# Kernel tuning notes

Hardware: AMD Instinct MI355X
Metric: run time of the kernel (lower is better)

The kernel has to match this reference:

```python
import jax, jax.numpy as jnp
import numpy as np

# dims: d_model D, d_inner DI=2*D, d_state S, dt_rank R, conv kernel K, layers NL
D, DI, S, R, K, NL = 512, 1024, 16, 32, 4, 6
B, L = 4, 1024
EPS = 1e-5


def _ln(x, w, b):
    m = x.mean(-1, keepdims=True)
    v = ((x - m) ** 2).mean(-1, keepdims=True)
    return (x - m) * jax.lax.rsqrt(v + EPS) * w + b


def _causal_conv(x, w, b):
    # depthwise causal conv1d: x [B,L,DI], w [DI,K], left-pad K-1 (matches Conv1d(padding=K-1) then crop)
    xp = jnp.pad(x, ((0, 0), (K - 1, 0), (0, 0)))
    y = sum(xp[:, k:k + x.shape[1], :] * w[:, k] for k in range(K))
    return y + b


def _mamba(h, in_w, cw, cb, xp_w, dt_w, dt_b, A_log, Dp, out_w):
    # h: [B,L,D]
    xz = jnp.einsum('bld,ed->ble', h, in_w)        # [B,L,2*DI]
    x, z = jnp.split(xz, 2, axis=-1)
    x = jax.nn.silu(_causal_conv(x, cw, cb))       # [B,L,DI]
    dbc = jnp.einsum('bld,ed->ble', x, xp_w)       # [B,L,R+2S]
    dt_r, Bm, Cm = dbc[..., :R], dbc[..., R:R + S], dbc[..., R + S:]
    dt = jax.nn.softplus(jnp.einsum('blr,dr->bld', dt_r, dt_w) + dt_b)  # [B,L,DI]
    A = -jnp.exp(A_log)                            # [DI,S]

    def step(hst, inp):
        dt_t, B_t, C_t, x_t = inp                  # [B,DI],[B,S],[B,S],[B,DI]
        dA = jnp.exp(dt_t[..., None] * A)          # [B,DI,S]
        hst = dA * hst + (dt_t * x_t)[..., None] * B_t[:, None, :]
        y = jnp.einsum('bds,bs->bd', hst, C_t)
        return hst, y

    h0 = jnp.zeros((x.shape[0], DI, S), x.dtype)
    xs = (dt.transpose(1, 0, 2), Bm.transpose(1, 0, 2), Cm.transpose(1, 0, 2), x.transpose(1, 0, 2))
    _, ys = jax.lax.scan(step, h0, xs)
    y = ys.transpose(1, 0, 2) + x * Dp
    y = y * jax.nn.silu(z)
    return jnp.einsum('bld,ed->ble', y, out_w)     # [B,L,D]


def setup_inputs() -> dict:
    key = jax.random.key(0)
    ks = jax.random.split(key, 10)
    n = lambda k, shp, s: s * jax.random.normal(k, shp, jnp.float32)
    inp = {}
    inp['xs_pad'] = jax.random.normal(ks[0], (B, L, D), jnp.float32)
    inp['ilens'] = jax.random.randint(ks[1], (B,), 1, L + 1)
    inp['norm_w'] = jnp.ones((NL, D), jnp.float32)
    inp['norm_b'] = jnp.zeros((NL, D), jnp.float32)
    inp['in_proj_w'] = n(ks[2], (NL, 2 * DI, D), 0.02)
    inp['conv_w'] = n(ks[3], (NL, DI, K), 0.1)
    inp['conv_b'] = jnp.zeros((NL, DI), jnp.float32)
    inp['x_proj_w'] = n(ks[4], (NL, R + 2 * S, DI), 0.02)
    inp['dt_proj_w'] = n(ks[5], (NL, DI, R), 0.1)
    inp['dt_proj_b'] = n(ks[6], (NL, DI), 0.01)
    inp['A_log'] = jnp.log(jnp.broadcast_to(jnp.arange(1, S + 1, dtype=jnp.float32), (NL, DI, S)))
    inp['D_param'] = jnp.ones((NL, DI), jnp.float32)
    inp['out_proj_w'] = n(ks[7], (NL, D, DI), 0.02)
    inp['normf_w'] = jnp.ones((D,), jnp.float32)
    inp['normf_b'] = jnp.zeros((D,), jnp.float32)
    inp['after_w'] = jnp.ones((D,), jnp.float32)
    inp['after_b'] = jnp.zeros((D,), jnp.float32)
    return inp


def reference(xs_pad, ilens, norm_w, norm_b, in_proj_w, conv_w, conv_b, x_proj_w,
              dt_proj_w, dt_proj_b, A_log, D_param, out_proj_w,
              normf_w, normf_b, after_w, after_b):
    hidden = xs_pad
    residual = None
    for i in range(NL):
        residual = hidden + residual if residual is not None else hidden
        hn = _ln(residual, norm_w[i], norm_b[i])
        hidden = _mamba(hn, in_proj_w[i], conv_w[i], conv_b[i], x_proj_w[i],
                        dt_proj_w[i], dt_proj_b[i], A_log[i], D_param[i], out_proj_w[i])
    residual = hidden + residual
    out = _ln(residual, normf_w, normf_b)   # norm_f
    out = _ln(out, after_w, after_b)        # after_norm (normalize_before=True)
    olens = jnp.minimum(ilens, L)
    return out, olens
```

## Files before the change

kernel.cpp:

```cpp
#include <hip/hip_runtime.h>
#include <hip/hip_bf16.h>
#include <math.h>

#define D_   512
#define DI_  1024
#define S_   16
#define R_   32
#define KC_  4
#define NL_  6
#define B_   4
#define L_   1024
#define BL_  (B_*L_)
#define NC_  64
#define CL_  (L_/NC_)
#define BDI_ (B_*DI_)
#define LOG2E 1.44269504f
#define SKX  8
#define SKO  4

typedef __hip_bfloat16 bf16;
typedef __attribute__((ext_vector_type(8))) short bf16x8;
typedef __attribute__((ext_vector_type(4))) float f32x4;
typedef unsigned short u16;

#define QIDX(s, c, bd) (((size_t)(s) * NC_ + (c)) * BDI_ + (bd))

__device__ __forceinline__ float b2f(u16 u) {
  union { unsigned int i; float f; } x; x.i = ((unsigned int)u) << 16; return x.f;
}

__device__ __forceinline__ u16 f2bu(float f) {
  bf16 h = __float2bfloat16(f);
  return *(u16*)&h;
}

__device__ __forceinline__ float softplus_f(float v) {
  float e = __expf(-fabsf(v));
  return fmaxf(v, 0.f) + __logf(1.f + e);
}

__device__ __forceinline__ void gload16(const void* g, void* l) {
  __builtin_amdgcn_global_load_lds((const __attribute__((address_space(1))) void*)g,
                                   (__attribute__((address_space(3))) void*)l, 16, 0, 0);
}

#define N1_ (NL_*2*DI_*D_)
#define N2_ (N1_ + NL_*D_*DI_)
#define N3_ (N2_ + NL_*128*DI_)
#define N4_ (N3_ + NL_*DI_)
__global__ void setup_k(const float* __restrict__ in_w, const float* __restrict__ out_w,
                        const float* __restrict__ xp_w, const float* __restrict__ A_log,
                        bf16* __restrict__ inw_b, bf16* __restrict__ outw_b,
                        bf16* __restrict__ xpw_b,
                        float* __restrict__ an2b, float* __restrict__ ff,
                        float* __restrict__ an2f) {
  for (int i = blockIdx.x * blockDim.x + threadIdx.x; i < N4_; i += gridDim.x * blockDim.x) {
    if (i < N1_) {
      inw_b[i] = __float2bfloat16(in_w[i]);
    } else if (i < N2_) {
      int j = i - N1_;
      outw_b[j] = __float2bfloat16(out_w[j]);
    } else if (i < N3_) {
      int j = i - N2_;
      int c = j & (DI_ - 1);
      int r = (j >> 10) & 127;
      int l = j >> 17;
      float v = (r < 64) ? xp_w[((size_t)l * 64 + r) * DI_ + c] : 0.f;
      xpw_b[j] = __float2bfloat16(v);
    } else {
      int j = i - N3_;
      int d = j & (DI_ - 1);
      int l = j >> 10;
      float base = -expf(A_log[(size_t)j * S_]) * LOG2E;
      bool fast = true;
      #pragma unroll
      for (int s = 0; s < S_; ++s) {
        float a = -expf(A_log[(size_t)j * S_ + s]) * LOG2E;
        an2f[((size_t)l * S_ + s) * DI_ + d] = a;
        fast = fast && (fabsf(a - (float)(s + 1) * base) <= 1e-5f * fabsf(a));
      }
      an2b[j] = base;
      ff[j] = fast ? 1.f : 0.f;
    }
  }
}

__global__ __launch_bounds__(128) void addln_k(
    const float* __restrict__ x0, const u16* __restrict__ parts,
    u16* __restrict__ resid, const float* __restrict__ w, const float* __restrict__ b,
    bf16* __restrict__ hn, int first)
{
  __shared__ float red[4];
  const int row = blockIdx.x, t = threadIdx.x;
  const int lane = t & 63, wv = t >> 6;
  const size_t o = (size_t)row * D_ + t * 4;
  float4 v;
  if (first) {
    v = *(const float4*)(x0 + o);
  } else {
    const size_t ps = (size_t)BL_ * D_;
    v.x = 0.f; v.y = 0.f; v.z = 0.f; v.w = 0.f;
    #pragma unroll
    for (int p = 0; p < SKO; ++p) {
      ushort4 q = *(const ushort4*)(parts + p * ps + o);
      v.x += b2f(q.x); v.y += b2f(q.y); v.z += b2f(q.z); v.w += b2f(q.w);
    }
    ushort4 r = *(const ushort4*)(resid + o);
    v.x += b2f(r.x); v.y += b2f(r.y); v.z += b2f(r.z); v.w += b2f(r.w);
  }
  {
    ushort4 rw;
    rw.x = f2bu(v.x); rw.y = f2bu(v.y); rw.z = f2bu(v.z); rw.w = f2bu(v.w);
    *(ushort4*)(resid + o) = rw;
  }
  float s = v.x + v.y + v.z + v.w;
  float ss = v.x*v.x + v.y*v.y + v.z*v.z + v.w*v.w;
  #pragma unroll
  for (int o2 = 32; o2 > 0; o2 >>= 1) { s += __shfl_xor(s, o2); ss += __shfl_xor(ss, o2); }
  if (lane == 0) { red[wv * 2] = s; red[wv * 2 + 1] = ss; }
  __syncthreads();
  float S = red[0] + red[2], SS = red[1] + red[3];
  float m = S * (1.f / D_), var = SS * (1.f / D_) - m * m;
  float rs = rsqrtf(var + 1e-5f);
  float4 w4 = *(const float4*)(w + t * 4);
  float4 b4 = *(const float4*)(b + t * 4);
  bf16* o8 = hn + o;
  o8[0] = __float2bfloat16((v.x - m) * rs * w4.x + b4.x);
  o8[1] = __float2bfloat16((v.y - m) * rs * w4.y + b4.y);
  o8[2] = __float2bfloat16((v.z - m) * rs * w4.z + b4.z);
  o8[3] = __float2bfloat16((v.w - m) * rs * w4.w + b4.w);
}

__global__ __launch_bounds__(256) void gemm_bt(
    const bf16* __restrict__ A, int lda,
    const bf16* __restrict__ B, int ldb,
    bf16* __restrict__ Cb,
    int K, int Nact, int M, int epi)
{
  __shared__ __align__(16) bf16 As[128 * 32];
  __shared__ __align__(16) bf16 Bs[128 * 32];
  const int tid = threadIdx.x;
  const int wave = tid >> 6, lane = tid & 63;
  const int bm = blockIdx.x * 128, bn = blockIdx.y * 128;
  const int kz = blockIdx.z;
  const int Kc = K / gridDim.z;
  const int k0 = kz * Kc, k1 = k0 + Kc;
  const int wr = (wave >> 1) << 6, wc = (wave & 1) << 6;
  const int srow = lane >> 2, scg = lane & 3;
  const int rA = lane & 15, kq = (lane >> 4) << 3;
  f32x4 acc[4][4] = {};
  for (int kt = k0; kt < k1; kt += 32) {
    __syncthreads();
    #pragma unroll
    for (int p = 0; p < 2; ++p) {
      int chunk = wave * 2 + p;
      int row = (chunk << 4) + srow;
      gload16(A + (size_t)(bm + row) * lda + kt + scg * 8, &As[chunk * 512]);
      gload16(B + (size_t)(bn + row) * ldb + kt + scg * 8, &Bs[chunk * 512]);
    }
    __syncthreads();
    bf16x8 af[4], bq[4];
    #pragma unroll
    for (int m = 0; m < 4; ++m) af[m] = *(const bf16x8*)&As[(wr + m * 16 + rA) * 32 + kq];
    #pragma unroll
    for (int n = 0; n < 4; ++n) bq[n] = *(const bf16x8*)&Bs[(wc + n * 16 + rA) * 32 + kq];
    #pragma unroll
    for (int m = 0; m < 4; ++m)
      #pragma unroll
      for (int n = 0; n < 4; ++n)
        acc[m][n] = __builtin_amdgcn_mfma_f32_16x16x32_bf16(af[m], bq[n], acc[m][n], 0, 0, 0);
  }
  const int cr = (lane >> 4) << 2, cc = lane & 15;
  const size_t pbase = (epi == 1) ? (size_t)kz * M * Nact : 0;
  #pragma unroll
  for (int m = 0; m < 4; ++m)
    #pragma unroll
    for (int n = 0; n < 4; ++n) {
      int col = bn + wc + n * 16 + cc;
      if (col >= Nact) continue;
      #pragma unroll
      for (int j = 0; j < 4; ++j) {
        size_t row = (size_t)(bm + wr + m * 16 + cr + j);
        Cb[pbase + row * Nact + col] = __float2bfloat16(acc[m][n][j]);
      }
    }
}

__global__ __launch_bounds__(256) void conv_silu_k(
    const u16* __restrict__ xz, const float* __restrict__ cw, const float* __restrict__ cb,
    bf16* __restrict__ xcb)
{
  int g = blockIdx.x * 256 + threadIdx.x;
  int dq = g & (DI_ / 8 - 1);
  int bl = g >> 7;
  int l = bl & (L_ - 1), b = bl >> 10;
  int d = dq * 8;
  float a[8], wv[8][KC_];
  #pragma unroll
  for (int e = 0; e < 8; ++e) {
    float4 w4 = *(const float4*)(cw + (d + e) * KC_);
    wv[e][0] = w4.x; wv[e][1] = w4.y; wv[e][2] = w4.z; wv[e][3] = w4.w;
    a[e] = cb[d + e];
  }
  #pragma unroll
  for (int k = 0; k < KC_; ++k) {
    int lt = l + k - 3;
    if (lt < 0) continue;
    bf16x8 xv = *(const bf16x8*)(xz + (size_t)(b * L_ + lt) * (2 * DI_) + d);
    #pragma unroll
    for (int e = 0; e < 8; ++e) a[e] += b2f((u16)xv[e]) * wv[e][k];
  }
  bf16 o8[8];
  #pragma unroll
  for (int e = 0; e < 8; ++e) {
    float v = a[e] / (1.f + __expf(-a[e]));
    o8[e] = __float2bfloat16(v);
  }
  *(bf16x8*)(xcb + (size_t)bl * DI_ + d) = *(const bf16x8*)o8;
}


__global__ __launch_bounds__(256) void scanA_k(
    const u16* __restrict__ x, const u16* __restrict__ xpart,
    const float* __restrict__ dtw, const float* __restrict__ dtbias,
    const float* __restrict__ A_log, const float* __restrict__ an2b,
    const float* __restrict__ ff, float* __restrict__ sumdt,
    bf16* __restrict__ q, bf16* __restrict__ dtb, float* __restrict__ dbcC)
{
  __shared__ float SM[CL_ * 48];
  const int tid = threadIdx.x;
  int g = blockIdx.x * 256 + tid;
  int d = g & (DI_ - 1);
  int cb = g >> 10;
  int b = cb & (B_ - 1);
  int c = cb >> 2;
  const int quarter = blockIdx.x & 3;
  {
    const size_t ps = (size_t)BL_ * 64;
    for (int idx = tid; idx < CL_ * 48; idx += 256) {
      int row = idx / 48, col = idx - row * 48;
      size_t rb = ((size_t)(b * L_ + c * CL_ + row)) * 64 + col;
      float v = 0.f;
      #pragma unroll
      for (int p = 0; p < SKX; ++p) v += b2f(xpart[p * ps + rb]);
      SM[idx] = v;
    }
    if (quarter == 0) {
      for (int idx = tid; idx < CL_ * 32; idx += 256) {
        int row = idx >> 5, col = idx & 31;
        size_t rb = ((size_t)(b * L_ + c * CL_ + row)) * 64 + 32 + col;
        float v = 0.f;
        #pragma unroll
        for (int p = 0; p < SKX; ++p) v += b2f(xpart[p * ps + rb]);
        dbcC[((size_t)(b * L_ + c * CL_ + row)) * 32 + col] = v;
      }
    }
  }
  float wv[R_];
  #pragma unroll
  for (int r = 0; r < R_; r += 4) {
    float4 w4 = *(const float4*)(dtw + (size_t)d * R_ + r);
    wv[r] = w4.x; wv[r + 1] = w4.y; wv[r + 2] = w4.z; wv[r + 3] = w4.w;
  }
  const float bias = dtbias[d];
  const float An2b = an2b[d];
  const bool fast = (ff[d] != 0.f);
  __syncthreads();
  float h[S_] = {};
  float sdt = 0.f;
  const size_t base = ((size_t)b * L_ + c * CL_) * DI_ + d;
  float cx = b2f(x[base]);
  float dtv;
  {
    float v = bias;
    #pragma unroll
    for (int r = 0; r < R_; r += 4) {
      float4 dv = *(const float4*)&SM[r];
      v += dv.x * wv[r] + dv.y * wv[r + 1] + dv.z * wv[r + 2] + dv.w * wv[r + 3];
    }
    dtv = softplus_f(v);
  }
  for (int i = 0; i < CL_; ++i) {
    const int ip = (i + 1 < CL_) ? i + 1 : i;
    float nx = b2f(x[base + (size_t)ip * DI_]);
    float vn = bias;
    #pragma unroll
    for (int r = 0; r < R_; r += 4) {
      float4 dv = *(const float4*)&SM[ip * 48 + r];
      vn += dv.x * wv[r] + dv.y * wv[r + 1] + dv.z * wv[r + 2] + dv.w * wv[r + 3];
    }
    dtb[base + (size_t)i * DI_] = __float2bfloat16(dtv);
    sdt += dtv;
    float u = dtv * cx;
    float Bv[S_];
    *(float4*)&Bv[0]  = *(const float4*)&SM[i * 48 + 32];
    *(float4*)&Bv[4]  = *(const float4*)&SM[i * 48 + 36];
    *(float4*)&Bv[8]  = *(const float4*)&SM[i * 48 + 40];
    *(float4*)&Bv[12] = *(const float4*)&SM[i * 48 + 44];
    float da[S_];
    if (fast) {
      float E1 = exp2f(dtv * An2b);
      float E2 = E1 * E1;
      float E4 = E2 * E2;
      da[0] = E1; da[1] = E2; da[2] = E2 * E1; da[3] = E4;
      #pragma unroll
      for (int s = 4; s < S_; ++s) da[s] = da[s - 4] * E4;
    } else {
      #pragma unroll
      for (int s = 0; s < S_; ++s)
        da[s] = exp2f(dtv * (-expf(A_log[(size_t)d * S_ + s]) * LOG2E));
    }
    #pragma unroll
    for (int s = 0; s < S_; ++s) h[s] = da[s] * h[s] + u * Bv[s];
    dtv = softplus_f(vn);
    cx = nx;
  }
  int bd = b * DI_ + d;
  sumdt[(size_t)c * BDI_ + bd] = sdt;
  #pragma unroll
  for (int s = 0; s < S_; ++s) q[QIDX(s, c, bd)] = __float2bfloat16(h[s]);
}

__global__ __launch_bounds__(256) void scanB_k(
    const float* __restrict__ sumdt, const u16* __restrict__ q,
    const float* __restrict__ an2f, bf16* __restrict__ hi)
{
  int g = blockIdx.x * 256 + threadIdx.x;
  int s = g >> 12;
  int bd = g & (BDI_ - 1);
  int d = bd & (DI_ - 1);
  float An2 = an2f[(size_t)s * DI_ + d];
  float h = 0.f;
  float sd = sumdt[bd];
  float qq = b2f(q[(size_t)s * NC_ * BDI_ + bd]);
  for (int c = 0; c < NC_; ++c) {
    float sdn = sd, qn = qq;
    if (c + 1 < NC_) {
      sdn = sumdt[(size_t)(c + 1) * BDI_ + bd];
      qn  = b2f(q[QIDX(s, c + 1, bd)]);
    }
    hi[QIDX(s, c, bd)] = __float2bfloat16(h);
    h = exp2f(An2 * sd) * h + qq;
    sd = sdn; qq = qn;
  }
}

__global__ __launch_bounds__(256) void scanC_k(
    const u16* __restrict__ dt, const u16* __restrict__ x, const float* __restrict__ dbcC,
    const float* __restrict__ A_log, const float* __restrict__ an2b,
    const float* __restrict__ ff, const float* __restrict__ Dp, const u16* __restrict__ xz,
    const u16* __restrict__ hi, bf16* __restrict__ y)
{
  __shared__ float BCS[CL_ * 32];
  const int tid = threadIdx.x;
  int g = blockIdx.x * 256 + tid;
  int d = g & (DI_ - 1);
  int cb = g >> 10;
  int b = cb & (B_ - 1);
  int c = cb >> 2;
  {
    int f = tid * 2;
    int step = f >> 5, off = f & 31;
    float2 v = *(const float2*)(dbcC + ((size_t)(b * L_ + c * CL_ + step)) * 32 + off);
    BCS[f] = v.x; BCS[f + 1] = v.y;
  }
  const float An2b = an2b[d];
  const bool fast = (ff[d] != 0.f);
  int bd = b * DI_ + d;
  float h[S_];
  #pragma unroll
  for (int s = 0; s < S_; ++s) h[s] = b2f(hi[QIDX(s, c, bd)]);
  __syncthreads();
  float dpv = Dp[d];
  const size_t rid0 = (size_t)b * L_ + c * CL_;
  const size_t base = rid0 * DI_ + d;
  float cdt = b2f(dt[base]), cx = b2f(x[base]);
  float cz = b2f(xz[rid0 * (2 * DI_) + DI_ + d]);
  float Ecur = exp2f(cdt * An2b);
  for (int i = 0; i < CL_; ++i) {
    const int ip = (i + 1 < CL_) ? i + 1 : i;
    float ndt = b2f(dt[base + (size_t)ip * DI_]);
    float nx  = b2f(x[base + (size_t)ip * DI_]);
    float nz  = b2f(xz[(rid0 + ip) * (2 * DI_) + DI_ + d]);
    float Enext = exp2f(ndt * An2b);
    float u = cdt * cx;
    float Bv[S_], Cv[S_];
    *(float4*)&Bv[0]  = *(const float4*)&BCS[i * 32 + 0];
    *(float4*)&Bv[4]  = *(const float4*)&BCS[i * 32 + 4];
    *(float4*)&Bv[8]  = *(const float4*)&BCS[i * 32 + 8];
    *(float4*)&Bv[12] = *(const float4*)&BCS[i * 32 + 12];
    *(float4*)&Cv[0]  = *(const float4*)&BCS[i * 32 + 16];
    *(float4*)&Cv[4]  = *(const float4*)&BCS[i * 32 + 20];
    *(float4*)&Cv[8]  = *(const float4*)&BCS[i * 32 + 24];
    *(float4*)&Cv[12] = *(const float4*)&BCS[i * 32 + 28];
    float da[S_];
    if (fast) {
      float E1 = Ecur;
      float E2 = E1 * E1;
      float E4 = E2 * E2;
      da[0] = E1; da[1] = E2; da[2] = E2 * E1; da[3] = E4;
      #pragma unroll
      for (int s = 4; s < S_; ++s) da[s] = da[s - 4] * E4;
    } else {
      #pragma unroll
      for (int s = 0; s < S_; ++s)
        da[s] = exp2f(cdt * (-expf(A_log[(size_t)d * S_ + s]) * LOG2E));
    }
    float acc = 0.f;
    #pragma unroll
    for (int s = 0; s < S_; ++s) {
      h[s] = da[s] * h[s] + u * Bv[s];
      acc += h[s] * Cv[s];
    }
    acc += cx * dpv;
    acc *= cz / (1.f + __expf(-cz));
    y[(rid0 + i) * DI_ + d] = __float2bfloat16(acc);
    cdt = ndt; cx = nx; cz = nz; Ecur = Enext;
  }
}

__global__ __launch_bounds__(128) void final_k(
    const u16* __restrict__ parts, const u16* __restrict__ res,
    const float* __restrict__ fw, const float* __restrict__ fb,
    const float* __restrict__ aw, const float* __restrict__ ab,
    const int* __restrict__ ilens, float* __restrict__ out, int outN)
{
  __shared__ float red[4];
  const int row = blockIdx.x, t = threadIdx.x;
  const int lane = t & 63, wv = t >> 6;
  const size_t ps = (size_t)BL_ * D_;
  const size_t o0 = (size_t)row * D_ + t * 4;
  float4 v; v.x = 0.f; v.y = 0.f; v.z = 0.f; v.w = 0.f;
  #pragma unroll
  for (int p = 0; p < SKO; ++p) {
    ushort4 q = *(const ushort4*)(parts + p * ps + o0);
    v.x += b2f(q.x); v.y += b2f(q.y); v.z += b2f(q.z); v.w += b2f(q.w);
  }
  ushort4 r = *(const ushort4*)(res + o0);
  v.x += b2f(r.x); v.y += b2f(r.y); v.z += b2f(r.z); v.w += b2f(r.w);
  float s = v.x + v.y + v.z + v.w;
  float ss = v.x*v.x + v.y*v.y + v.z*v.z + v.w*v.w;
  #pragma unroll
  for (int o = 32; o > 0; o >>= 1) { s += __shfl_xor(s, o); ss += __shfl_xor(ss, o); }
  if (lane == 0) { red[wv * 2] = s; red[wv * 2 + 1] = ss; }
  __syncthreads();
  float S = red[0] + red[2], SS = red[1] + red[3];
  float m = S * (1.f / D_), var = SS * (1.f / D_) - m * m;
  float rs = rsqrtf(var + 1e-5f);
  float4 w4 = *(const float4*)(fw + t * 4);
  float4 b4 = *(const float4*)(fb + t * 4);
  float4 x1;
  x1.x = (v.x - m) * rs * w4.x + b4.x;
  x1.y = (v.y - m) * rs * w4.y + b4.y;
  x1.z = (v.z - m) * rs * w4.z + b4.z;
  x1.w = (v.w - m) * rs * w4.w + b4.w;
  __syncthreads();
  float s2 = x1.x + x1.y + x1.z + x1.w;
  float ss2 = x1.x*x1.x + x1.y*x1.y + x1.z*x1.z + x1.w*x1.w;
  #pragma unroll
  for (int o = 32; o > 0; o >>= 1) { s2 += __shfl_xor(s2, o); ss2 += __shfl_xor(ss2, o); }
  if (lane == 0) { red[wv * 2] = s2; red[wv * 2 + 1] = ss2; }
  __syncthreads();
  float S2 = red[0] + red[2], SS2 = red[1] + red[3];
  float m2 = S2 * (1.f / D_), var2 = SS2 * (1.f / D_) - m2 * m2;
  float rs2 = rsqrtf(var2 + 1e-5f);
  float4 aw4 = *(const float4*)(aw + t * 4);
  float4 ab4 = *(const float4*)(ab + t * 4);
  float4 o;
  o.x = (x1.x - m2) * rs2 * aw4.x + ab4.x;
  o.y = (x1.y - m2) * rs2 * aw4.y + ab4.y;
  o.z = (x1.z - m2) * rs2 * aw4.z + ab4.z;
  o.w = (x1.w - m2) * rs2 * aw4.w + ab4.w;
  *(float4*)(out + (size_t)row * D_ + t * 4) = o;
  if (row == 0 && t < B_) {
    int q = ilens[t];
    out[outN + t] = (float)(q < L_ ? q : L_);
  }
}

extern "C" void kernel_launch(void* const* d_in, const int* in_sizes, int n_in,
                              void* d_out, int out_size, void* d_ws, size_t ws_size,
                              hipStream_t stream) {
  const float* xs     = (const float*)d_in[0];
  const int*   ilens  = (const int*)d_in[1];
  const float* norm_w = (const float*)d_in[2];
  const float* norm_b = (const float*)d_in[3];
  const float* in_w   = (const float*)d_in[4];
  const float* conv_w = (const float*)d_in[5];
  const float* conv_b = (const float*)d_in[6];
  const float* xp_w   = (const float*)d_in[7];
  const float* dt_w   = (const float*)d_in[8];
  const float* dt_b   = (const float*)d_in[9];
  const float* A_log  = (const float*)d_in[10];
  const float* Dp     = (const float*)d_in[11];
  const float* out_w  = (const float*)d_in[12];
  const float* nfw    = (const float*)d_in[13];
  const float* nfb    = (const float*)d_in[14];
  const float* afw    = (const float*)d_in[15];
  const float* afb    = (const float*)d_in[16];
  float* out = (float*)d_out;

  char* ws = (char*)d_ws;
  size_t off = 0;
  auto alloc = [&](size_t bytes) -> char* {
    char* p = ws + off;
    off += (bytes + 255) & ~(size_t)255;
    return p;
  };
  bf16*  inw_b  = (bf16*)alloc((size_t)NL_ * 2 * DI_ * D_ * 2);
  bf16*  outw_b = (bf16*)alloc((size_t)NL_ * D_ * DI_ * 2);
  bf16*  xpw_b  = (bf16*)alloc((size_t)NL_ * 128 * DI_ * 2);
  float* an2b   = (float*)alloc((size_t)NL_ * DI_ * 4);
  float* ffb    = (float*)alloc((size_t)NL_ * DI_ * 4);
  float* an2f   = (float*)alloc((size_t)NL_ * S_ * DI_ * 4);
  u16*   resid  = (u16*)alloc((size_t)BL_ * D_ * 2);
  bf16*  hn_b   = (bf16*)alloc((size_t)BL_ * D_ * 2);
  bf16*  xzb    = (bf16*)alloc((size_t)BL_ * 2 * DI_ * 2);
  bf16*  xcb    = (bf16*)alloc((size_t)BL_ * DI_ * 2);
  bf16*  xpart  = (bf16*)alloc((size_t)SKX * BL_ * 64 * 2);
  float* dbcC   = (float*)alloc((size_t)BL_ * 32 * 4);
  bf16*  dtb    = (bf16*)alloc((size_t)BL_ * DI_ * 2);
  float* sdt    = (float*)alloc((size_t)NC_ * BDI_ * 4);
  bf16*  qb     = (bf16*)alloc((size_t)S_ * NC_ * BDI_ * 2);
  bf16*  hini   = (bf16*)alloc((size_t)S_ * NC_ * BDI_ * 2);
  bf16*  yb     = (bf16*)alloc((size_t)BL_ * DI_ * 2);
  bf16*  opart  = (bf16*)alloc((size_t)SKO * BL_ * D_ * 2);
  if (off > ws_size) return;

  setup_k<<<4096, 256, 0, stream>>>(in_w, out_w, xp_w, A_log,
                                    inw_b, outw_b, xpw_b, an2b, ffb, an2f);

  for (int i = 0; i < NL_; ++i) {
    addln_k<<<BL_, 128, 0, stream>>>(xs, (const u16*)opart, resid,
                                     norm_w + i * D_, norm_b + i * D_, hn_b, i == 0);
    dim3 g1(32, 16, 1);
    gemm_bt<<<g1, 256, 0, stream>>>(hn_b, D_, inw_b + (size_t)i * 2 * DI_ * D_, D_,
                                    xzb, D_, 2 * DI_, BL_, 3);
    conv_silu_k<<<(BL_ * DI_ / 8) / 256, 256, 0, stream>>>(
        (const u16*)xzb, conv_w + i * DI_ * KC_, conv_b + i * DI_, xcb);
    dim3 g2(32, 1, SKX);
    gemm_bt<<<g2, 256, 0, stream>>>(xcb, DI_, xpw_b + (size_t)i * 128 * DI_, DI_,
                                    xpart, DI_, 64, BL_, 1);
    scanA_k<<<(NC_ * B_ * DI_) / 256, 256, 0, stream>>>(
        (const u16*)xcb, (const u16*)xpart, dt_w + (size_t)i * DI_ * R_, dt_b + i * DI_,
        A_log + (size_t)i * DI_ * S_, an2b + i * DI_, ffb + i * DI_, sdt, qb, dtb, dbcC);
    scanB_k<<<(B_ * DI_ * S_) / 256, 256, 0, stream>>>(
        sdt, (const u16*)qb, an2f + (size_t)i * S_ * DI_, hini);
    scanC_k<<<(NC_ * B_ * DI_) / 256, 256, 0, stream>>>(
        (const u16*)dtb, (const u16*)xcb, dbcC, A_log + (size_t)i * DI_ * S_,
        an2b + i * DI_, ffb + i * DI_, Dp + i * DI_,
        (const u16*)xzb, (const u16*)hini, yb);
    dim3 g4(32, 4, SKO);
    gemm_bt<<<g4, 256, 0, stream>>>(yb, DI_, outw_b + (size_t)i * D_ * DI_, DI_,
                                    opart, DI_, D_, BL_, 1);
  }
  final_k<<<BL_, 128, 0, stream>>>((const u16*)opart, resid, nfw, nfb, afw, afb, ilens, out,
                                   out_size - B_);
}
```

Baseline: 717.8 us.

## Split scan state dimension across thread pairs in scanA and scanC

Each channel's 16-entry SSM state in the chunked scan kernels is now split across two adjacent threads, eight states each, with 512-thread blocks. The dt projection dot product and the C-weighted output sum are combined with a lane-xor shuffle. This doubles the thread count and halves per-thread registers and serial work, aiming at better latency hiding in the sequential per-chunk loop. The cost is redundant per-thread loads of x, dt and z, an extra shuffle every step, and half the threads sitting idle during stores.

Result: slower. 749.1 us (+4.4%).

```diff
diff --git a/kernel.cpp b/kernel.cpp
--- a/kernel.cpp
+++ b/kernel.cpp
@@ -220,7 +220,7 @@
 }
 
 
-__global__ __launch_bounds__(256) void scanA_k(
+__global__ __launch_bounds__(512) void scanA_k(
     const u16* __restrict__ x, const u16* __restrict__ xpart,
     const float* __restrict__ dtw, const float* __restrict__ dtbias,
     const float* __restrict__ A_log, const float* __restrict__ an2b,
@@ -229,7 +229,8 @@
 {
   __shared__ float SM[CL_ * 48];
   const int tid = threadIdx.x;
-  int g = blockIdx.x * 256 + tid;
+  const int half = tid & 1;
+  int g = blockIdx.x * 256 + (tid >> 1);
   int d = g & (DI_ - 1);
   int cb = g >> 10;
   int b = cb & (B_ - 1);
@@ -237,7 +238,7 @@
   const int quarter = blockIdx.x & 3;
   {
     const size_t ps = (size_t)BL_ * 64;
-    for (int idx = tid; idx < CL_ * 48; idx += 256) {
+    for (int idx = tid; idx < CL_ * 48; idx += 512) {
       int row = idx / 48, col = idx - row * 48;
       size_t rb = ((size_t)(b * L_ + c * CL_ + row)) * 64 + col;
       float v = 0.f;
@@ -246,7 +247,7 @@
       SM[idx] = v;
     }
     if (quarter == 0) {
-      for (int idx = tid; idx < CL_ * 32; idx += 256) {
+      for (int idx = tid; idx < CL_ * 32; idx += 512) {
         int row = idx >> 5, col = idx & 31;
         size_t rb = ((size_t)(b * L_ + c * CL_ + row)) * 64 + 32 + col;
         float v = 0.f;
@@ -256,17 +257,17 @@
       }
     }
   }
-  float wv[R_];
-  #pragma unroll
-  for (int r = 0; r < R_; r += 4) {
-    float4 w4 = *(const float4*)(dtw + (size_t)d * R_ + r);
+  float wv[16];
+  #pragma unroll
+  for (int r = 0; r < 16; r += 4) {
+    float4 w4 = *(const float4*)(dtw + (size_t)d * R_ + half * 16 + r);
     wv[r] = w4.x; wv[r + 1] = w4.y; wv[r + 2] = w4.z; wv[r + 3] = w4.w;
   }
-  const float bias = dtbias[d];
+  const float bias = half ? 0.f : dtbias[d];
   const float An2b = an2b[d];
   const bool fast = (ff[d] != 0.f);
   __syncthreads();
-  float h[S_] = {};
+  float h[8] = {};
   float sdt = 0.f;
   const size_t base = ((size_t)b * L_ + c * CL_) * DI_ + d;
   float cx = b2f(x[base]);
@@ -274,10 +275,11 @@
   {
     float v = bias;
     #pragma unroll
-    for (int r = 0; r < R_; r += 4) {
-      float4 dv = *(const float4*)&SM[r];
+    for (int r = 0; r < 16; r += 4) {
+      float4 dv = *(const float4*)&SM[half * 16 + r];
       v += dv.x * wv[r] + dv.y * wv[r + 1] + dv.z * wv[r + 2] + dv.w * wv[r + 3];
     }
+    v += __shfl_xor(v, 1);
     dtv = softplus_f(v);
   }
   for (int i = 0; i < CL_; ++i) {
@@ -285,40 +287,38 @@
     float nx = b2f(x[base + (size_t)ip * DI_]);
     float vn = bias;
     #pragma unroll
-    for (int r = 0; r < R_; r += 4) {
-      float4 dv = *(const float4*)&SM[ip * 48 + r];
+    for (int r = 0; r < 16; r += 4) {
+      float4 dv = *(const float4*)&SM[ip * 48 + half * 16 + r];
       vn += dv.x * wv[r] + dv.y * wv[r + 1] + dv.z * wv[r + 2] + dv.w * wv[r + 3];
     }
-    dtb[base + (size_t)i * DI_] = __float2bfloat16(dtv);
+    if (half == 0) dtb[base + (size_t)i * DI_] = __float2bfloat16(dtv);
     sdt += dtv;
     float u = dtv * cx;
-    float Bv[S_];
-    *(float4*)&Bv[0]  = *(const float4*)&SM[i * 48 + 32];
-    *(float4*)&Bv[4]  = *(const float4*)&SM[i * 48 + 36];
-    *(float4*)&Bv[8]  = *(const float4*)&SM[i * 48 + 40];
-    *(float4*)&Bv[12] = *(const float4*)&SM[i * 48 + 44];
-    float da[S_];
+    float Bv[8];
+    *(float4*)&Bv[0] = *(const float4*)&SM[i * 48 + 32 + half * 8];
+    *(float4*)&Bv[4] = *(const float4*)&SM[i * 48 + 36 + half * 8];
+    float da[8];
     if (fast) {
       float E1 = exp2f(dtv * An2b);
-      float E2 = E1 * E1;
-      float E4 = E2 * E2;
-      da[0] = E1; da[1] = E2; da[2] = E2 * E1; da[3] = E4;
-      #pragma unroll
-      for (int s = 4; s < S_; ++s) da[s] = da[s - 4] * E4;
+      float E2 = E1 * E1, E4 = E2 * E2, E8 = E4 * E4;
+      float bs = half ? E8 : 1.f;
+      da[0] = bs * E1;      da[1] = bs * E2;      da[2] = bs * E2 * E1; da[3] = bs * E4;
+      da[4] = bs * E4 * E1; da[5] = bs * E4 * E2; da[6] = da[5] * E1;   da[7] = bs * E8;
     } else {
       #pragma unroll
-      for (int s = 0; s < S_; ++s)
-        da[s] = exp2f(dtv * (-expf(A_log[(size_t)d * S_ + s]) * LOG2E));
-    }
-    #pragma unroll
-    for (int s = 0; s < S_; ++s) h[s] = da[s] * h[s] + u * Bv[s];
+      for (int j = 0; j < 8; ++j)
+        da[j] = exp2f(dtv * (-expf(A_log[(size_t)d * S_ + half * 8 + j]) * LOG2E));
+    }
+    #pragma unroll
+    for (int j = 0; j < 8; ++j) h[j] = da[j] * h[j] + u * Bv[j];
+    vn += __shfl_xor(vn, 1);
     dtv = softplus_f(vn);
     cx = nx;
   }
   int bd = b * DI_ + d;
-  sumdt[(size_t)c * BDI_ + bd] = sdt;
-  #pragma unroll
-  for (int s = 0; s < S_; ++s) q[QIDX(s, c, bd)] = __float2bfloat16(h[s]);
+  if (half == 0) sumdt[(size_t)c * BDI_ + bd] = sdt;
+  #pragma unroll
+  for (int j = 0; j < 8; ++j) q[QIDX(half * 8 + j, c, bd)] = __float2bfloat16(h[j]);
 }
 
 __global__ __launch_bounds__(256) void scanB_k(
@@ -345,7 +345,7 @@
   }
 }
 
-__global__ __launch_bounds__(256) void scanC_k(
+__global__ __launch_bounds__(512) void scanC_k(
     const u16* __restrict__ dt, const u16* __restrict__ x, const float* __restrict__ dbcC,
     const float* __restrict__ A_log, const float* __restrict__ an2b,
     const float* __restrict__ ff, const float* __restrict__ Dp, const u16* __restrict__ xz,
@@ -353,23 +353,22 @@
 {
   __shared__ float BCS[CL_ * 32];
   const int tid = threadIdx.x;
-  int g = blockIdx.x * 256 + tid;
+  const int half = tid & 1;
+  int g = blockIdx.x * 256 + (tid >> 1);
   int d = g & (DI_ - 1);
   int cb = g >> 10;
   int b = cb & (B_ - 1);
   int c = cb >> 2;
   {
-    int f = tid * 2;
-    int step = f >> 5, off = f & 31;
-    float2 v = *(const float2*)(dbcC + ((size_t)(b * L_ + c * CL_ + step)) * 32 + off);
-    BCS[f] = v.x; BCS[f + 1] = v.y;
+    int row = tid >> 5, col = tid & 31;
+    BCS[tid] = dbcC[((size_t)(b * L_ + c * CL_ + row)) * 32 + col];
   }
   const float An2b = an2b[d];
   const bool fast = (ff[d] != 0.f);
   int bd = b * DI_ + d;
-  float h[S_];
-  #pragma unroll
-  for (int s = 0; s < S_; ++s) h[s] = b2f(hi[QIDX(s, c, bd)]);
+  float h[8];
+  #pragma unroll
+  for (int j = 0; j < 8; ++j) h[j] = b2f(hi[QIDX(half * 8 + j, c, bd)]);
   __syncthreads();
   float dpv = Dp[d];
   const size_t rid0 = (size_t)b * L_ + c * CL_;
@@ -384,37 +383,35 @@
     float nz  = b2f(xz[(rid0 + ip) * (2 * DI_) + DI_ + d]);
     float Enext = exp2f(ndt * An2b);
     float u = cdt * cx;
-    float Bv[S_], Cv[S_];
-    *(float4*)&Bv[0]  = *(const float4*)&BCS[i * 32 + 0];
-    *(float4*)&Bv[4]  = *(const float4*)&BCS[i * 32 + 4];
-    *(float4*)&Bv[8]  = *(const float4*)&BCS[i * 32 + 8];
-    *(float4*)&Bv[12] = *(const float4*)&BCS[i * 32 + 12];
-    *(float4*)&Cv[0]  = *(const float4*)&BCS[i * 32 + 16];
-    *(float4*)&Cv[4]  = *(const float4*)&BCS[i * 32 + 20];
-    *(float4*)&Cv[8]  = *(const float4*)&BCS[i * 32 + 24];
-    *(float4*)&Cv[12] = *(const float4*)&BCS[i * 32 + 28];
-    float da[S_];
+    float Bv[8], Cv[8];
+    *(float4*)&Bv[0] = *(const float4*)&BCS[i * 32 + half * 8];
+    *(float4*)&Bv[4] = *(const float4*)&BCS[i * 32 + 4 + half * 8];
+    *(float4*)&Cv[0] = *(const float4*)&BCS[i * 32 + 16 + half * 8];
+    *(float4*)&Cv[4] = *(const float4*)&BCS[i * 32 + 20 + half * 8];
+    float da[8];
     if (fast) {
       float E1 = Ecur;
-      float E2 = E1 * E1;
-      float E4 = E2 * E2;
-      da[0] = E1; da[1] = E2; da[2] = E2 * E1; da[3] = E4;
-      #pragma unroll
-      for (int s = 4; s < S_; ++s) da[s] = da[s - 4] * E4;
+      float E2 = E1 * E1, E4 = E2 * E2, E8 = E4 * E4;
+      float bs = half ? E8 : 1.f;
+      da[0] = bs * E1;      da[1] = bs * E2;      da[2] = bs * E2 * E1; da[3] = bs * E4;
+      da[4] = bs * E4 * E1; da[5] = bs * E4 * E2; da[6] = da[5] * E1;   da[7] = bs * E8;
     } else {
       #pragma unroll
-      for (int s = 0; s < S_; ++s)
-        da[s] = exp2f(cdt * (-expf(A_log[(size_t)d * S_ + s]) * LOG2E));
+      for (int j = 0; j < 8; ++j)
+        da[j] = exp2f(cdt * (-expf(A_log[(size_t)d * S_ + half * 8 + j]) * LOG2E));
     }
     float acc = 0.f;
     #pragma unroll
-    for (int s = 0; s < S_; ++s) {
-      h[s] = da[s] * h[s] + u * Bv[s];
-      acc += h[s] * Cv[s];
-    }
-    acc += cx * dpv;
-    acc *= cz / (1.f + __expf(-cz));
-    y[(rid0 + i) * DI_ + d] = __float2bfloat16(acc);
+    for (int j = 0; j < 8; ++j) {
+      h[j] = da[j] * h[j] + u * Bv[j];
+      acc += h[j] * Cv[j];
+    }
+    acc += __shfl_xor(acc, 1);
+    if (half == 0) {
+      acc += cx * dpv;
+      acc *= cz / (1.f + __expf(-cz));
+      y[(rid0 + i) * DI_ + d] = __float2bfloat16(acc);
+    }
     cdt = ndt; cx = nx; cz = nz; Ecur = Enext;
   }
 }
@@ -541,12 +538,12 @@
     dim3 g2(32, 1, SKX);
     gemm_bt<<<g2, 256, 0, stream>>>(xcb, DI_, xpw_b + (size_t)i * 128 * DI_, DI_,
                                     xpart, DI_, 64, BL_, 1);
-    scanA_k<<<(NC_ * B_ * DI_) / 256, 256, 0, stream>>>(
+    scanA_k<<<(NC_ * B_ * DI_) / 256, 512, 0, stream>>>(
         (const u16*)xcb, (const u16*)xpart, dt_w + (size_t)i * DI_ * R_, dt_b + i * DI_,
         A_log + (size_t)i * DI_ * S_, an2b + i * DI_, ffb + i * DI_, sdt, qb, dtb, dbcC);
     scanB_k<<<(B_ * DI_ * S_) / 256, 256, 0, stream>>>(
         sdt, (const u16*)qb, an2f + (size_t)i * S_ * DI_, hini);
-    scanC_k<<<(NC_ * B_ * DI_) / 256, 256, 0, stream>>>(
+    scanC_k<<<(NC_ * B_ * DI_) / 256, 512, 0, stream>>>(
         (const u16*)dtb, (const u16*)xcb, dbcC, A_log + (size_t)i * DI_ * S_,
         an2b + i * DI_, ffb + i * DI_, Dp + i * DI_,
         (const u16*)xzb, (const u16*)hini, yb);
```

## Compute local chunk output in scan pass A; replace second scan with correction pass

Applied to the files above, without the earlier changes.

The first chunked scan pass now also produces the chunk-local output y (h·C plus the D skip term) and the running cumulative dt per step. The third pass no longer re-runs the recurrence. It adds a correction term from the chunk's initial state, decayed by exp(cumdt·A) and dotted with C, then applies the SiLU(z) gate. This removes a second 16-state recurrence per element, at the cost of an extra bf16 buffer write and read and cumulative dt stored in bf16, which may lose precision.

New measurement: 735.9 us. +2.5%, slower.

```diff
diff --git a/kernel.cpp b/kernel.cpp
--- a/kernel.cpp
+++ b/kernel.cpp
@@ -224,10 +224,11 @@
     const u16* __restrict__ x, const u16* __restrict__ xpart,
     const float* __restrict__ dtw, const float* __restrict__ dtbias,
     const float* __restrict__ A_log, const float* __restrict__ an2b,
-    const float* __restrict__ ff, float* __restrict__ sumdt,
-    bf16* __restrict__ q, bf16* __restrict__ dtb, float* __restrict__ dbcC)
-{
-  __shared__ float SM[CL_ * 48];
+    const float* __restrict__ ff, const float* __restrict__ Dp,
+    float* __restrict__ sumdt, bf16* __restrict__ q,
+    bf16* __restrict__ ct, bf16* __restrict__ yl, float* __restrict__ dbcC)
+{
+  __shared__ float SM[CL_ * 64];
   const int tid = threadIdx.x;
   int g = blockIdx.x * 256 + tid;
   int d = g & (DI_ - 1);
@@ -237,23 +238,16 @@
   const int quarter = blockIdx.x & 3;
   {
     const size_t ps = (size_t)BL_ * 64;
-    for (int idx = tid; idx < CL_ * 48; idx += 256) {
-      int row = idx / 48, col = idx - row * 48;
+    for (int vi = 0; vi < 4; ++vi) {
+      int idx = vi * 256 + tid;
+      int row = idx >> 6, col = idx & 63;
       size_t rb = ((size_t)(b * L_ + c * CL_ + row)) * 64 + col;
       float v = 0.f;
       #pragma unroll
       for (int p = 0; p < SKX; ++p) v += b2f(xpart[p * ps + rb]);
       SM[idx] = v;
-    }
-    if (quarter == 0) {
-      for (int idx = tid; idx < CL_ * 32; idx += 256) {
-        int row = idx >> 5, col = idx & 31;
-        size_t rb = ((size_t)(b * L_ + c * CL_ + row)) * 64 + 32 + col;
-        float v = 0.f;
-        #pragma unroll
-        for (int p = 0; p < SKX; ++p) v += b2f(xpart[p * ps + rb]);
-        dbcC[((size_t)(b * L_ + c * CL_ + row)) * 32 + col] = v;
-      }
+      if (quarter == 0 && col >= 32)
+        dbcC[((size_t)(b * L_ + c * CL_ + row)) * 32 + (col - 32)] = v;
     }
   }
   float wv[R_];
@@ -265,6 +259,7 @@
   const float bias = dtbias[d];
   const float An2b = an2b[d];
   const bool fast = (ff[d] != 0.f);
+  const float dpv = Dp[d];
   __syncthreads();
   float h[S_] = {};
   float sdt = 0.f;
@@ -286,17 +281,21 @@
     float vn = bias;
     #pragma unroll
     for (int r = 0; r < R_; r += 4) {
-      float4 dv = *(const float4*)&SM[ip * 48 + r];
+      float4 dv = *(const float4*)&SM[ip * 64 + r];
       vn += dv.x * wv[r] + dv.y * wv[r + 1] + dv.z * wv[r + 2] + dv.w * wv[r + 3];
     }
-    dtb[base + (size_t)i * DI_] = __float2bfloat16(dtv);
     sdt += dtv;
+    ct[base + (size_t)i * DI_] = __float2bfloat16(sdt);
     float u = dtv * cx;
-    float Bv[S_];
-    *(float4*)&Bv[0]  = *(const float4*)&SM[i * 48 + 32];
-    *(float4*)&Bv[4]  = *(const float4*)&SM[i * 48 + 36];
-    *(float4*)&Bv[8]  = *(const float4*)&SM[i * 48 + 40];
-    *(float4*)&Bv[12] = *(const float4*)&SM[i * 48 + 44];
+    float Bv[S_], Cv[S_];
+    *(float4*)&Bv[0]  = *(const float4*)&SM[i * 64 + 32];
+    *(float4*)&Bv[4]  = *(const float4*)&SM[i * 64 + 36];
+    *(float4*)&Bv[8]  = *(const float4*)&SM[i * 64 + 40];
+    *(float4*)&Bv[12] = *(const float4*)&SM[i * 64 + 44];
+    *(float4*)&Cv[0]  = *(const float4*)&SM[i * 64 + 48];
+    *(float4*)&Cv[4]  = *(const float4*)&SM[i * 64 + 52];
+    *(float4*)&Cv[8]  = *(const float4*)&SM[i * 64 + 56];
+    *(float4*)&Cv[12] = *(const float4*)&SM[i * 64 + 60];
     float da[S_];
     if (fast) {
       float E1 = exp2f(dtv * An2b);
@@ -310,8 +309,14 @@
       for (int s = 0; s < S_; ++s)
         da[s] = exp2f(dtv * (-expf(A_log[(size_t)d * S_ + s]) * LOG2E));
     }
-    #pragma unroll
-    for (int s = 0; s < S_; ++s) h[s] = da[s] * h[s] + u * Bv[s];
+    float acc = 0.f;
+    #pragma unroll
+    for (int s = 0; s < S_; ++s) {
+      h[s] = da[s] * h[s] + u * Bv[s];
+      acc += h[s] * Cv[s];
+    }
+    acc += cx * dpv;
+    yl[base + (size_t)i * DI_] = __float2bfloat16(acc);
     dtv = softplus_f(vn);
     cx = nx;
   }
@@ -345,13 +350,13 @@
   }
 }
 
-__global__ __launch_bounds__(256) void scanC_k(
-    const u16* __restrict__ dt, const u16* __restrict__ x, const float* __restrict__ dbcC,
+__global__ __launch_bounds__(256) void corrC_k(
+    const u16* __restrict__ ct, const u16* __restrict__ yl, const float* __restrict__ dbcC,
     const float* __restrict__ A_log, const float* __restrict__ an2b,
-    const float* __restrict__ ff, const float* __restrict__ Dp, const u16* __restrict__ xz,
+    const float* __restrict__ ff, const u16* __restrict__ xz,
     const u16* __restrict__ hi, bf16* __restrict__ y)
 {
-  __shared__ float BCS[CL_ * 32];
+  __shared__ float CS[CL_ * 16];
   const int tid = threadIdx.x;
   int g = blockIdx.x * 256 + tid;
   int d = g & (DI_ - 1);
@@ -359,43 +364,26 @@
   int b = cb & (B_ - 1);
   int c = cb >> 2;
   {
-    int f = tid * 2;
-    int step = f >> 5, off = f & 31;
-    float2 v = *(const float2*)(dbcC + ((size_t)(b * L_ + c * CL_ + step)) * 32 + off);
-    BCS[f] = v.x; BCS[f + 1] = v.y;
+    int row = tid >> 4, col = tid & 15;
+    CS[tid] = dbcC[((size_t)(b * L_ + c * CL_ + row)) * 32 + 16 + col];
   }
   const float An2b = an2b[d];
   const bool fast = (ff[d] != 0.f);
   int bd = b * DI_ + d;
-  float h[S_];
-  #pragma unroll
-  for (int s = 0; s < S_; ++s) h[s] = b2f(hi[QIDX(s, c, bd)]);
+  float hs[S_];
+  #pragma unroll
+  for (int s = 0; s < S_; ++s) hs[s] = b2f(hi[QIDX(s, c, bd)]);
   __syncthreads();
-  float dpv = Dp[d];
   const size_t rid0 = (size_t)b * L_ + c * CL_;
   const size_t base = rid0 * DI_ + d;
-  float cdt = b2f(dt[base]), cx = b2f(x[base]);
-  float cz = b2f(xz[rid0 * (2 * DI_) + DI_ + d]);
-  float Ecur = exp2f(cdt * An2b);
+  const size_t zb = rid0 * (2 * DI_) + DI_ + d;
   for (int i = 0; i < CL_; ++i) {
-    const int ip = (i + 1 < CL_) ? i + 1 : i;
-    float ndt = b2f(dt[base + (size_t)ip * DI_]);
-    float nx  = b2f(x[base + (size_t)ip * DI_]);
-    float nz  = b2f(xz[(rid0 + ip) * (2 * DI_) + DI_ + d]);
-    float Enext = exp2f(ndt * An2b);
-    float u = cdt * cx;
-    float Bv[S_], Cv[S_];
-    *(float4*)&Bv[0]  = *(const float4*)&BCS[i * 32 + 0];
-    *(float4*)&Bv[4]  = *(const float4*)&BCS[i * 32 + 4];
-    *(float4*)&Bv[8]  = *(const float4*)&BCS[i * 32 + 8];
-    *(float4*)&Bv[12] = *(const float4*)&BCS[i * 32 + 12];
-    *(float4*)&Cv[0]  = *(const float4*)&BCS[i * 32 + 16];
-    *(float4*)&Cv[4]  = *(const float4*)&BCS[i * 32 + 20];
-    *(float4*)&Cv[8]  = *(const float4*)&BCS[i * 32 + 24];
-    *(float4*)&Cv[12] = *(const float4*)&BCS[i * 32 + 28];
+    float cd  = b2f(ct[base + (size_t)i * DI_]);
+    float ylv = b2f(yl[base + (size_t)i * DI_]);
+    float zv  = b2f(xz[zb + (size_t)i * (2 * DI_)]);
     float da[S_];
     if (fast) {
-      float E1 = Ecur;
+      float E1 = exp2f(cd * An2b);
       float E2 = E1 * E1;
       float E4 = E2 * E2;
       da[0] = E1; da[1] = E2; da[2] = E2 * E1; da[3] = E4;
@@ -404,18 +392,14 @@
     } else {
       #pragma unroll
       for (int s = 0; s < S_; ++s)
-        da[s] = exp2f(cdt * (-expf(A_log[(size_t)d * S_ + s]) * LOG2E));
-    }
-    float acc = 0.f;
-    #pragma unroll
-    for (int s = 0; s < S_; ++s) {
-      h[s] = da[s] * h[s] + u * Bv[s];
-      acc += h[s] * Cv[s];
-    }
-    acc += cx * dpv;
-    acc *= cz / (1.f + __expf(-cz));
-    y[(rid0 + i) * DI_ + d] = __float2bfloat16(acc);
-    cdt = ndt; cx = nx; cz = nz; Ecur = Enext;
+        da[s] = exp2f(cd * (-expf(A_log[(size_t)d * S_ + s]) * LOG2E));
+    }
+    float corr = 0.f;
+    #pragma unroll
+    for (int s = 0; s < S_; ++s) corr += hs[s] * da[s] * CS[i * 16 + s];
+    float v = ylv + corr;
+    v *= zv / (1.f + __expf(-zv));
+    y[base + (size_t)i * DI_] = __float2bfloat16(v);
   }
 }
 
@@ -519,7 +503,8 @@
   bf16*  xcb    = (bf16*)alloc((size_t)BL_ * DI_ * 2);
   bf16*  xpart  = (bf16*)alloc((size_t)SKX * BL_ * 64 * 2);
   float* dbcC   = (float*)alloc((size_t)BL_ * 32 * 4);
-  bf16*  dtb    = (bf16*)alloc((size_t)BL_ * DI_ * 2);
+  bf16*  ctb    = (bf16*)alloc((size_t)BL_ * DI_ * 2);
+  bf16*  ylb    = (bf16*)alloc((size_t)BL_ * DI_ * 2);
   float* sdt    = (float*)alloc((size_t)NC_ * BDI_ * 4);
   bf16*  qb     = (bf16*)alloc((size_t)S_ * NC_ * BDI_ * 2);
   bf16*  hini   = (bf16*)alloc((size_t)S_ * NC_ * BDI_ * 2);
@@ -543,13 +528,13 @@
                                     xpart, DI_, 64, BL_, 1);
     scanA_k<<<(NC_ * B_ * DI_) / 256, 256, 0, stream>>>(
         (const u16*)xcb, (const u16*)xpart, dt_w + (size_t)i * DI_ * R_, dt_b + i * DI_,
-        A_log + (size_t)i * DI_ * S_, an2b + i * DI_, ffb + i * DI_, sdt, qb, dtb, dbcC);
+        A_log + (size_t)i * DI_ * S_, an2b + i * DI_, ffb + i * DI_, Dp + i * DI_,
+        sdt, qb, ctb, ylb, dbcC);
     scanB_k<<<(B_ * DI_ * S_) / 256, 256, 0, stream>>>(
         sdt, (const u16*)qb, an2f + (size_t)i * S_ * DI_, hini);
-    scanC_k<<<(NC_ * B_ * DI_) / 256, 256, 0, stream>>>(
-        (const u16*)dtb, (const u16*)xcb, dbcC, A_log + (size_t)i * DI_ * S_,
-        an2b + i * DI_, ffb + i * DI_, Dp + i * DI_,
-        (const u16*)xzb, (const u16*)hini, yb);
+    corrC_k<<<(NC_ * B_ * DI_) / 256, 256, 0, stream>>>(
+        (const u16*)ctb, (const u16*)ylb, dbcC, A_log + (size_t)i * DI_ * S_,
+        an2b + i * DI_, ffb + i * DI_, (const u16*)xzb, (const u16*)hini, yb);
     dim3 g4(32, 4, SKO);
     gemm_bt<<<g4, 256, 0, stream>>>(yb, DI_, outw_b + (size_t)i * D_ * DI_, DI_,
                                     opart, DI_, D_, BL_, 1);
```
